# Optimization experiments

Hardware: AMD Instinct MI355X
Metric: run time of the kernel (lower is better)

The kernel has to match this reference:

```python
import jax, jax.numpy as jnp
import numpy as np

C_PAIR = 128
N_TOK = 512
EPS = 1e-5


def _layernorm(x, w, b):
    mu = jnp.mean(x, axis=-1, keepdims=True)
    var = jnp.mean(jnp.square(x - mu), axis=-1, keepdims=True)
    return (x - mu) * jax.lax.rsqrt(var + EPS) * w + b


def setup_inputs() -> dict:
    key = jax.random.key(0)
    ks = jax.random.split(key, 8)
    c = C_PAIR
    pair = jax.random.normal(ks[0], (N_TOK, N_TOK, c), dtype=jnp.float32)
    mask = jax.random.uniform(ks[1], (N_TOK, N_TOK), dtype=jnp.float32)
    s_in = 1.0 / np.sqrt(c)
    W_proj = jax.random.normal(ks[2], (2 * c, c), dtype=jnp.float32) * s_in  # nn.Linear(c, 2c)
    W_gate = jax.random.normal(ks[3], (2 * c, c), dtype=jnp.float32) * s_in
    W_out = jax.random.normal(ks[4], (c, c), dtype=jnp.float32) * s_in
    W_glin = jax.random.normal(ks[5], (c, c), dtype=jnp.float32) * s_in
    ln1_w = jnp.ones((c,), jnp.float32)
    ln1_b = jnp.zeros((c,), jnp.float32)
    ln2_w = jnp.ones((c,), jnp.float32)
    ln2_b = jnp.zeros((c,), jnp.float32)
    return {"pair": pair, "mask": mask, "ln1_w": ln1_w, "ln1_b": ln1_b,
            "ln2_w": ln2_w, "ln2_b": ln2_b, "W_proj": W_proj, "W_gate": W_gate,
            "W_out": W_out, "W_glin": W_glin}


def reference(pair, mask, ln1_w, ln1_b, ln2_w, ln2_b, W_proj, W_gate, W_out, W_glin):
    # pair: [N, N, c], mask: [N, N]
    x = _layernorm(pair, ln1_w, ln1_b)
    input_pair = x
    proj = x @ W_proj.T                      # [N, N, 2c]
    proj = proj * mask[..., None]
    gate = x @ W_gate.T                      # [N, N, 2c]
    proj = proj * jax.nn.sigmoid(gate)
    # torch reshape(2c,...)->(c,2,...) then chunk: a = channels 0::2, b = channels 1::2
    a = proj[..., 0::2]                      # [N, N, c]
    b = proj[..., 1::2]                      # [N, N, c]
    # equation 'ckj,cki->cij' in channel-first == out[i,j,c] = sum_k a[k,j,c] * b[k,i,c]
    out = jnp.einsum('kjc,kic->ijc', a, b)   # [N, N, c]
    out = _layernorm(out, ln2_w, ln2_b)
    out = out @ W_out.T
    gate_out = input_pair @ W_glin.T
    return out * jax.nn.sigmoid(gate_out)
```

## Files before the change

kernel.cpp:

```cpp
#include <hip/hip_runtime.h>
#include <hip/hip_bf16.h>

using u16 = unsigned short;
typedef __attribute__((ext_vector_type(4))) float f32x4;
typedef __attribute__((ext_vector_type(8))) _Float16 f16x8;
typedef __attribute__((ext_vector_type(4))) unsigned short u16x4;

#define MFMA(a,b,c) __builtin_amdgcn_mfma_f32_16x16x32_f16((a),(b),(c),0,0,0)

__device__ __forceinline__ u16 f2h(float f){
  _Float16 h = (_Float16)f;
  return __builtin_bit_cast(u16, h);
}
__device__ __forceinline__ float sigm(float x){
  return 1.f / (1.f + __expf(-x));
}
__device__ __forceinline__ f16x8 ldw8(const float* __restrict__ W, int row, int koff){
  const float4* p = (const float4*)(W + row * 128 + koff);
  float4 f0 = p[0], f1 = p[1];
  f16x8 h;
  h[0] = (_Float16)f0.x; h[1] = (_Float16)f0.y; h[2] = (_Float16)f0.z; h[3] = (_Float16)f0.w;
  h[4] = (_Float16)f1.x; h[5] = (_Float16)f1.y; h[6] = (_Float16)f1.z; h[7] = (_Float16)f1.w;
  return h;
}

__launch_bounds__(256, 3)
__global__ void k1_ln_proj(const float* __restrict__ pair, const float* __restrict__ mask,
                           const float* __restrict__ ln1w, const float* __restrict__ ln1b,
                           const float* __restrict__ Wp, const float* __restrict__ Wg,
                           u16* __restrict__ a_r, u16* __restrict__ b_r){
  __shared__ float red_s[128], red_q[128], msk[128];
  __shared__ u16 xs[128 * 136];
  __shared__ u16 sbuf[4][16 * 132];
  int tid = threadIdx.x;
  int bid = blockIdx.x;
  int j   = bid >> 2;
  int k0  = (bid & 3) << 7;

  int cpos = tid & 31;
  int rsub = tid >> 5;
  float4 v[16];
  #pragma unroll
  for (int it = 0; it < 16; ++it){
    int kk = it * 8 + rsub;
    const float4* p = (const float4*)(pair + (((size_t)(k0 + kk) * 512 + j) << 7));
    v[it] = p[cpos];
    float s = v[it].x + v[it].y + v[it].z + v[it].w;
    float q = v[it].x*v[it].x + v[it].y*v[it].y + v[it].z*v[it].z + v[it].w*v[it].w;
    #pragma unroll
    for (int m = 16; m >= 1; m >>= 1){
      s += __shfl_xor(s, m);
      q += __shfl_xor(q, m);
    }
    if (cpos == 0){ red_s[kk] = s; red_q[kk] = q; }
  }
  if (tid < 128) msk[tid] = mask[(size_t)(k0 + tid) * 512 + j];
  __syncthreads();

  float4 w4 = ((const float4*)ln1w)[cpos];
  float4 b4 = ((const float4*)ln1b)[cpos];
  #pragma unroll
  for (int it = 0; it < 16; ++it){
    int kk = it * 8 + rsub;
    float mu = red_s[kk] * (1.f / 128.f);
    float var = red_q[kk] * (1.f / 128.f) - mu * mu;
    float rs = rsqrtf(var + 1e-5f);
    u16x4 o;
    o[0] = f2h((v[it].x - mu) * rs * w4.x + b4.x);
    o[1] = f2h((v[it].y - mu) * rs * w4.y + b4.y);
    o[2] = f2h((v[it].z - mu) * rs * w4.z + b4.z);
    o[3] = f2h((v[it].w - mu) * rs * w4.w + b4.w);
    *(u16x4*)&xs[kk * 136 + cpos * 4] = o;
  }
  __syncthreads();

  int lane = tid & 63;
  int wv   = tid >> 6;
  int l15  = lane & 15;
  int l4   = lane >> 4;
  u16* sb  = sbuf[wv];

  #pragma unroll
  for (int pi = 0; pi < 4; ++pi){
    int tp = pi * 4 + wv;
    int nP = tp * 16 + l15;
    f32x4 accP[8] = {}; f32x4 accG[8] = {};
    #pragma unroll
    for (int ks = 0; ks < 4; ++ks){
      f16x8 bP = ldw8(Wp, nP, ks * 32 + l4 * 8);
      f16x8 bG = ldw8(Wg, nP, ks * 32 + l4 * 8);
      #pragma unroll
      for (int mi = 0; mi < 8; ++mi){
        f16x8 af = *(const f16x8*)&xs[(mi * 16 + l15) * 136 + ks * 32 + l4 * 8];
        accP[mi] = MFMA(af, bP, accP[mi]);
        accG[mi] = MFMA(af, bG, accG[mi]);
      }
    }
    #pragma unroll
    for (int mi = 0; mi < 8; ++mi){
      int m0 = mi * 16 + l4 * 4;
      u16x4 o;
      #pragma unroll
      for (int r = 0; r < 4; ++r){
        float p = accP[mi][r] * msk[m0 + r] * sigm(accG[mi][r]);
        o[r] = f2h(p);
      }
      *(u16x4*)&sb[l15 * 132 + m0] = o;
    }
    #pragma unroll
    for (int r2 = 0; r2 < 8; ++r2){
      int row = r2 * 2 + (lane >> 5);
      int col = (lane & 31) * 4;
      u16x4 vv = *(const u16x4*)&sb[row * 132 + col];
      int nP2 = tp * 16 + row;
      int c = nP2 >> 1;
      u16* dst = (nP2 & 1) ? b_r : a_r;
      *(u16x4*)&dst[((size_t)c * 512 + j) * 512 + k0 + col] = vv;
    }
  }
}

__launch_bounds__(256, 2)
__global__ void k2_tri(const u16* __restrict__ a_r, const u16* __restrict__ b_r,
                       float* __restrict__ o_f){
  int tid = threadIdx.x;
  int p = blockIdx.x;
  int lb = (p & 7) * 256 + (p >> 3);
  int c  = lb >> 4;
  int t  = lb & 15;
  int lane = tid & 63, wv = tid >> 6;
  int i0 = (t >> 2) * 128 + (wv >> 1) * 64;
  int j0 = (t & 3) * 128 + (wv & 1) * 64;
  int l15 = lane & 15, l4 = lane >> 4;
  const u16* pa = a_r + (size_t)c * 262144;
  const u16* pb = b_r + (size_t)c * 262144;

  f32x4 acc[4][4] = {};
  for (int ks = 0; ks < 16; ++ks){
    f16x8 A[4], B[4];
    #pragma unroll
    for (int ai = 0; ai < 4; ++ai)
      A[ai] = *(const f16x8*)&pb[(i0 + ai * 16 + l15) * 512 + ks * 32 + l4 * 8];
    #pragma unroll
    for (int bj = 0; bj < 4; ++bj)
      B[bj] = *(const f16x8*)&pa[(j0 + bj * 16 + l15) * 512 + ks * 32 + l4 * 8];
    #pragma unroll
    for (int ai = 0; ai < 4; ++ai)
      #pragma unroll
      for (int bj = 0; bj < 4; ++bj)
        acc[ai][bj] = MFMA(A[ai], B[bj], acc[ai][bj]);
  }
  float* po = o_f + (size_t)c * 262144;
  #pragma unroll
  for (int ai = 0; ai < 4; ++ai){
    #pragma unroll
    for (int r = 0; r < 4; ++r){
      int i = i0 + ai * 16 + l4 * 4 + r;
      #pragma unroll
      for (int bj = 0; bj < 4; ++bj)
        po[i * 512 + j0 + bj * 16 + l15] = acc[ai][bj][r];
    }
  }
}

__launch_bounds__(256, 2)
__global__ void k3_out(const float* __restrict__ o_f, const float* __restrict__ pair,
                       const float* __restrict__ ln1w, const float* __restrict__ ln1b,
                       const float* __restrict__ ln2w, const float* __restrict__ ln2b,
                       const float* __restrict__ Wgl, const float* __restrict__ Wo,
                       float* __restrict__ out){
  __shared__ float ot[128 * 68];
  __shared__ u16 x1[64 * 136];
  __shared__ u16 x2[64 * 136];
  __shared__ float r1s[64], r1q[64];
  int tid = threadIdx.x, bid = blockIdx.x;
  int i  = bid >> 3;
  int j0 = (bid & 7) << 6;

  int cq = tid & 31, jsub = tid >> 5;
  float4 pv[8];
  #pragma unroll
  for (int it = 0; it < 8; ++it){
    int jj = it * 8 + jsub;
    const float4* p = (const float4*)(pair + (((size_t)i * 512 + j0 + jj) << 7));
    pv[it] = p[cq];
    float s = pv[it].x + pv[it].y + pv[it].z + pv[it].w;
    float q = pv[it].x*pv[it].x + pv[it].y*pv[it].y + pv[it].z*pv[it].z + pv[it].w*pv[it].w;
    #pragma unroll
    for (int m = 16; m >= 1; m >>= 1){
      s += __shfl_xor(s, m);
      q += __shfl_xor(q, m);
    }
    if (cq == 0){ r1s[jj] = s; r1q[jj] = q; }
  }
  __syncthreads();
  {
    float4 w1 = ((const float4*)ln1w)[cq];
    float4 b1 = ((const float4*)ln1b)[cq];
    #pragma unroll
    for (int it = 0; it < 8; ++it){
      int jj = it * 8 + jsub;
      float mu = r1s[jj] * (1.f / 128.f);
      float var = r1q[jj] * (1.f / 128.f) - mu * mu;
      float rs = rsqrtf(var + 1e-5f);
      u16x4 o;
      o[0] = f2h((pv[it].x - mu) * rs * w1.x + b1.x);
      o[1] = f2h((pv[it].y - mu) * rs * w1.y + b1.y);
      o[2] = f2h((pv[it].z - mu) * rs * w1.z + b1.z);
      o[3] = f2h((pv[it].w - mu) * rs * w1.w + b1.w);
      *(u16x4*)&x1[jj * 136 + cq * 4] = o;
    }
  }

  #pragma unroll
  for (int it = 0; it < 8; ++it){
    int f = it * 256 + tid;
    int cin = f >> 4, part = f & 15;
    float4 vld = *(const float4*)&o_f[(size_t)cin * 262144 + (size_t)i * 512 + j0 + part * 4];
    *(float4*)&ot[cin * 68 + part * 4] = vld;
  }
  __syncthreads();

  int jj2 = tid >> 2, qr = tid & 3;
  float s2 = 0.f, q2 = 0.f;
  #pragma unroll
  for (int u = 0; u < 32; ++u){
    float x = ot[(qr * 32 + u) * 68 + jj2];
    s2 += x; q2 += x * x;
  }
  s2 += __shfl_xor(s2, 1); q2 += __shfl_xor(q2, 1);
  s2 += __shfl_xor(s2, 2); q2 += __shfl_xor(q2, 2);
  float mu2 = s2 * (1.f / 128.f);
  float rs2 = rsqrtf(q2 * (1.f / 128.f) - mu2 * mu2 + 1e-5f);
  #pragma unroll
  for (int u = 0; u < 32; ++u){
    int cin = qr * 32 + u;
    float x = ot[cin * 68 + jj2];
    x2[jj2 * 136 + cin] = f2h((x - mu2) * rs2 * ln2w[cin] + ln2b[cin]);
  }
  __syncthreads();

  int lane = tid & 63, wv = tid >> 6;
  int l15 = lane & 15, l4 = lane >> 4;
  int n0 = wv * 32;
  f32x4 accO[4][2] = {};
  f32x4 accG[4][2] = {};
  #pragma unroll
  for (int ks = 0; ks < 4; ++ks){
    int koff = ks * 32 + l4 * 8;
    f16x8 B0 = ldw8(Wo, n0 + l15, koff);
    f16x8 B1 = ldw8(Wo, n0 + 16 + l15, koff);
    f16x8 G0 = ldw8(Wgl, n0 + l15, koff);
    f16x8 G1 = ldw8(Wgl, n0 + 16 + l15, koff);
    #pragma unroll
    for (int mi = 0; mi < 4; ++mi){
      f16x8 A2 = *(const f16x8*)&x2[(mi * 16 + l15) * 136 + koff];
      f16x8 A1 = *(const f16x8*)&x1[(mi * 16 + l15) * 136 + koff];
      accO[mi][0] = MFMA(A2, B0, accO[mi][0]);
      accO[mi][1] = MFMA(A2, B1, accO[mi][1]);
      accG[mi][0] = MFMA(A1, G0, accG[mi][0]);
      accG[mi][1] = MFMA(A1, G1, accG[mi][1]);
    }
  }
  #pragma unroll
  for (int mi = 0; mi < 4; ++mi){
    #pragma unroll
    for (int r = 0; r < 4; ++r){
      int m = mi * 16 + l4 * 4 + r;
      size_t tok = (size_t)i * 512 + j0 + m;
      #pragma unroll
      for (int nj = 0; nj < 2; ++nj){
        int cout = n0 + nj * 16 + l15;
        out[tok * 128 + cout] = accO[mi][nj][r] * sigm(accG[mi][nj][r]);
      }
    }
  }
}

extern "C" void kernel_launch(void* const* d_in, const int* in_sizes, int n_in,
                              void* d_out, int out_size, void* d_ws, size_t ws_size,
                              hipStream_t stream){
  (void)in_sizes; (void)n_in; (void)out_size; (void)ws_size;
  const float* pair = (const float*)d_in[0];
  const float* mask = (const float*)d_in[1];
  const float* ln1w = (const float*)d_in[2];
  const float* ln1b = (const float*)d_in[3];
  const float* ln2w = (const float*)d_in[4];
  const float* ln2b = (const float*)d_in[5];
  const float* Wp   = (const float*)d_in[6];
  const float* Wg   = (const float*)d_in[7];
  const float* Wo   = (const float*)d_in[8];
  const float* Wgl  = (const float*)d_in[9];
  float* out = (float*)d_out;

  char* ws = (char*)d_ws;
  u16*   a_r = (u16*)(ws);
  u16*   b_r = (u16*)(ws + 67108864);
  float* o_f = (float*)(ws + 134217728);

  hipLaunchKernelGGL(k1_ln_proj, dim3(2048), dim3(256), 0, stream, pair, mask, ln1w, ln1b, Wp, Wg, a_r, b_r);
  hipLaunchKernelGGL(k2_tri,     dim3(2048), dim3(256), 0, stream, a_r, b_r, o_f);
  hipLaunchKernelGGL(k3_out,     dim3(4096), dim3(256), 0, stream, o_f, pair, ln1w, ln1b, ln2w, ln2b, Wgl, Wo, out);
}
```

Before: 447.7 us.

## Split second layernorm and transpose into a separate kernel writing fp16 token-major

Moves the second layernorm and the channel-major to token-major transpose out of the output kernel into a new kernel. That kernel writes an fp16 token-major buffer, reusing the a_r workspace region. The output kernel now loads its A operand straight from global memory, which frees the shared-memory staging and lets occupancy rise to 4 blocks per SM. In exchange it adds a kernel launch and an extra global round trip (a 64 MB fp16 write plus read).

After: 451.6 us. No clear change (+0.9%).

```diff
diff --git a/kernel.cpp b/kernel.cpp
--- a/kernel.cpp
+++ b/kernel.cpp
@@ -5,6 +5,7 @@
 typedef __attribute__((ext_vector_type(4))) float f32x4;
 typedef __attribute__((ext_vector_type(8))) _Float16 f16x8;
 typedef __attribute__((ext_vector_type(4))) unsigned short u16x4;
+typedef __attribute__((ext_vector_type(8))) unsigned short u16x8;
 
 #define MFMA(a,b,c) __builtin_amdgcn_mfma_f32_16x16x32_f16((a),(b),(c),0,0,0)
 
@@ -163,15 +164,78 @@
   }
 }
 
-__launch_bounds__(256, 2)
-__global__ void k3_out(const float* __restrict__ o_f, const float* __restrict__ pair,
+__launch_bounds__(256, 4)
+__global__ void k2b_lnt(const float* __restrict__ o_f,
+                        const float* __restrict__ ln2w, const float* __restrict__ ln2b,
+                        u16* __restrict__ x2g){
+  __shared__ float sred[2][4][16][4];
+  __shared__ float mu_s[64], rs_s[64];
+  __shared__ u16 tr2[64 * 132];
+  int tid = threadIdx.x;
+  size_t t0 = (size_t)blockIdx.x * 64;
+  int part = tid & 15;
+  int grp  = tid >> 4;
+  int wv = tid >> 6, lane = tid & 63;
+
+  f32x4 vals[8];
+  float s4[4] = {0,0,0,0}, q4[4] = {0,0,0,0};
+  #pragma unroll
+  for (int it = 0; it < 8; ++it){
+    int ci = it * 16 + grp;
+    vals[it] = *(const f32x4*)&o_f[(size_t)ci * 262144 + t0 + part * 4];
+    #pragma unroll
+    for (int r = 0; r < 4; ++r){ s4[r] += vals[it][r]; q4[r] += vals[it][r]*vals[it][r]; }
+  }
+  #pragma unroll
+  for (int r = 0; r < 4; ++r){
+    s4[r] += __shfl_xor(s4[r], 16); q4[r] += __shfl_xor(q4[r], 16);
+    s4[r] += __shfl_xor(s4[r], 32); q4[r] += __shfl_xor(q4[r], 32);
+  }
+  if (lane < 16){
+    #pragma unroll
+    for (int r = 0; r < 4; ++r){ sred[0][wv][lane][r] = s4[r]; sred[1][wv][lane][r] = q4[r]; }
+  }
+  __syncthreads();
+  if (tid < 64){
+    float s = 0.f, q = 0.f;
+    #pragma unroll
+    for (int w = 0; w < 4; ++w){ s += sred[0][w][tid >> 2][tid & 3]; q += sred[1][w][tid >> 2][tid & 3]; }
+    float mu = s * (1.f / 128.f);
+    float var = q * (1.f / 128.f) - mu * mu;
+    mu_s[tid] = mu;
+    rs_s[tid] = rsqrtf(var + 1e-5f);
+  }
+  __syncthreads();
+  #pragma unroll
+  for (int it = 0; it < 8; ++it){
+    int ci = it * 16 + grp;
+    float w2 = ln2w[ci], b2 = ln2b[ci];
+    #pragma unroll
+    for (int r = 0; r < 4; ++r){
+      int tl = part * 4 + r;
+      tr2[tl * 132 + ci] = f2h((vals[it][r] - mu_s[tl]) * rs_s[tl] * w2 + b2);
+    }
+  }
+  __syncthreads();
+  #pragma unroll
+  for (int it = 0; it < 4; ++it){
+    int flat = it * 256 + tid;
+    int t = flat >> 4, ch = flat & 15;
+    u16x4 lo = *(const u16x4*)&tr2[t * 132 + ch * 8];
+    u16x4 hi = *(const u16x4*)&tr2[t * 132 + ch * 8 + 4];
+    u16x8 o;
+    o[0]=lo[0]; o[1]=lo[1]; o[2]=lo[2]; o[3]=lo[3];
+    o[4]=hi[0]; o[5]=hi[1]; o[6]=hi[2]; o[7]=hi[3];
+    *(u16x8*)&x2g[(t0 + t) * 128 + ch * 8] = o;
+  }
+}
+
+__launch_bounds__(256, 4)
+__global__ void k3_out(const u16* __restrict__ x2g, const float* __restrict__ pair,
                        const float* __restrict__ ln1w, const float* __restrict__ ln1b,
-                       const float* __restrict__ ln2w, const float* __restrict__ ln2b,
                        const float* __restrict__ Wgl, const float* __restrict__ Wo,
                        float* __restrict__ out){
-  __shared__ float ot[128 * 68];
   __shared__ u16 x1[64 * 136];
-  __shared__ u16 x2[64 * 136];
   __shared__ float r1s[64], r1q[64];
   int tid = threadIdx.x, bid = blockIdx.x;
   int i  = bid >> 3;
@@ -211,33 +275,6 @@
       *(u16x4*)&x1[jj * 136 + cq * 4] = o;
     }
   }
-
-  #pragma unroll
-  for (int it = 0; it < 8; ++it){
-    int f = it * 256 + tid;
-    int cin = f >> 4, part = f & 15;
-    float4 vld = *(const float4*)&o_f[(size_t)cin * 262144 + (size_t)i * 512 + j0 + part * 4];
-    *(float4*)&ot[cin * 68 + part * 4] = vld;
-  }
-  __syncthreads();
-
-  int jj2 = tid >> 2, qr = tid & 3;
-  float s2 = 0.f, q2 = 0.f;
-  #pragma unroll
-  for (int u = 0; u < 32; ++u){
-    float x = ot[(qr * 32 + u) * 68 + jj2];
-    s2 += x; q2 += x * x;
-  }
-  s2 += __shfl_xor(s2, 1); q2 += __shfl_xor(q2, 1);
-  s2 += __shfl_xor(s2, 2); q2 += __shfl_xor(q2, 2);
-  float mu2 = s2 * (1.f / 128.f);
-  float rs2 = rsqrtf(q2 * (1.f / 128.f) - mu2 * mu2 + 1e-5f);
-  #pragma unroll
-  for (int u = 0; u < 32; ++u){
-    int cin = qr * 32 + u;
-    float x = ot[cin * 68 + jj2];
-    x2[jj2 * 136 + cin] = f2h((x - mu2) * rs2 * ln2w[cin] + ln2b[cin]);
-  }
   __syncthreads();
 
   int lane = tid & 63, wv = tid >> 6;
@@ -254,7 +291,7 @@
     f16x8 G1 = ldw8(Wgl, n0 + 16 + l15, koff);
     #pragma unroll
     for (int mi = 0; mi < 4; ++mi){
-      f16x8 A2 = *(const f16x8*)&x2[(mi * 16 + l15) * 136 + koff];
+      f16x8 A2 = *(const f16x8*)&x2g[((size_t)i * 512 + j0 + mi * 16 + l15) * 128 + koff];
       f16x8 A1 = *(const f16x8*)&x1[(mi * 16 + l15) * 136 + koff];
       accO[mi][0] = MFMA(A2, B0, accO[mi][0]);
       accO[mi][1] = MFMA(A2, B1, accO[mi][1]);
@@ -297,8 +334,10 @@
   u16*   a_r = (u16*)(ws);
   u16*   b_r = (u16*)(ws + 67108864);
   float* o_f = (float*)(ws + 134217728);
+  u16*   x2g = (u16*)(ws);
 
   hipLaunchKernelGGL(k1_ln_proj, dim3(2048), dim3(256), 0, stream, pair, mask, ln1w, ln1b, Wp, Wg, a_r, b_r);
   hipLaunchKernelGGL(k2_tri,     dim3(2048), dim3(256), 0, stream, a_r, b_r, o_f);
-  hipLaunchKernelGGL(k3_out,     dim3(4096), dim3(256), 0, stream, o_f, pair, ln1w, ln1b, ln2w, ln2b, Wgl, Wo, out);
-}
+  hipLaunchKernelGGL(k2b_lnt,    dim3(4096), dim3(256), 0, stream, o_f, ln2w, ln2b, x2g);
+  hipLaunchKernelGGL(k3_out,     dim3(4096), dim3(256), 0, stream, x2g, pair, ln1w, ln1b, Wgl, Wo, out);
+}
```
